# Performance work log

Measured on AMD Instinct MI355X. Metric: run time of the kernel, lower is better.

## Reference

```python
import jax, jax.numpy as jnp
import numpy as np
from jax import lax

D_MODEL = 512
D_STATE = 64
D_CONV = 4
EXPAND = 2
HEADDIM = 64
D_INNER = EXPAND * D_MODEL          # 1024
NHEADS = D_INNER // HEADDIM         # 16
CONV_DIM = D_INNER + 2 * D_STATE    # 1152 (x, B, C go through depthwise conv)
D_PROJ = 2 * D_INNER + 2 * D_STATE + NHEADS  # 2192
EPS = 1e-5


def silu(x):
    return x * jax.nn.sigmoid(x)


def layernorm(x, w, b):
    mu = jnp.mean(x, axis=-1, keepdims=True)
    var = jnp.mean((x - mu) ** 2, axis=-1, keepdims=True)
    return (x - mu) * lax.rsqrt(var + EPS) * w + b


def mamba2(x, in_w, conv_w, conv_b, dt_bias, A_log, D_h, mnorm_w, out_w):
    """Faithful Mamba2 forward (sequential selective-scan form of SSD).
    x: [B, L, D_MODEL]"""
    Bsz, L, _ = x.shape
    zxbcdt = x @ in_w  # [B, L, D_PROJ]
    z = zxbcdt[..., :D_INNER]
    xBC = zxbcdt[..., D_INNER:D_INNER + CONV_DIM]
    dt = zxbcdt[..., -NHEADS:]

    # causal depthwise conv1d over sequence, then SiLU
    xBC_pad = jnp.pad(xBC, ((0, 0), (D_CONV - 1, 0), (0, 0)))
    xBC = lax.conv_general_dilated(
        xBC_pad, conv_w, window_strides=(1,), padding='VALID',
        dimension_numbers=('NWC', 'WIO', 'NWC'), feature_group_count=CONV_DIM)
    xBC = silu(xBC + conv_b)

    xh = xBC[..., :D_INNER].reshape(Bsz, L, NHEADS, HEADDIM)      # [B,L,H,P]
    Bc = xBC[..., D_INNER:D_INNER + D_STATE]                      # [B,L,N]
    Cc = xBC[..., D_INNER + D_STATE:]                             # [B,L,N]

    dt = jax.nn.softplus(dt + dt_bias)          # [B,L,H]
    dA = jnp.exp(dt * (-jnp.exp(A_log)))        # [B,L,H]
    dtx = dt[..., None] * xh                    # [B,L,H,P]

    def step(h, ins):
        dA_t, dtx_t, B_t, C_t = ins  # [B,H], [B,H,P], [B,N], [B,N]
        h = h * dA_t[:, :, None, None] + dtx_t[..., None] * B_t[:, None, None, :]
        y = jnp.einsum('bhpn,bn->bhp', h, C_t)
        return h, y

    h0 = jnp.zeros((Bsz, NHEADS, HEADDIM, D_STATE), x.dtype)
    xs = (jnp.moveaxis(dA, 1, 0), jnp.moveaxis(dtx, 1, 0),
          jnp.moveaxis(Bc, 1, 0), jnp.moveaxis(Cc, 1, 0))
    _, ys = lax.scan(step, h0, xs)              # [L,B,H,P]
    y = jnp.moveaxis(ys, 0, 1) + D_h[None, None, :, None] * xh
    y = y.reshape(Bsz, L, D_INNER)

    # gated RMSNorm: rmsnorm(y * silu(z)) * weight
    g = y * silu(z)
    g = g * lax.rsqrt(jnp.mean(g * g, axis=-1, keepdims=True) + EPS) * mnorm_w
    return g @ out_w  # [B, L, D_MODEL]


def setup_inputs() -> dict:
    key = jax.random.key(0)
    ks = jax.random.split(key, 16)
    B, L = 2, 4096
    s = 0.02
    inp = {
        'x': jax.random.normal(ks[0], (B, L, D_MODEL), jnp.float32),
        'norm_in_w': jnp.ones((D_MODEL,), jnp.float32),
        'norm_in_b': jnp.zeros((D_MODEL,), jnp.float32),
        'norm_out_w': jnp.ones((D_MODEL,), jnp.float32),
        'norm_out_b': jnp.zeros((D_MODEL,), jnp.float32),
        'in_w': jax.random.normal(ks[1], (D_MODEL, D_PROJ), jnp.float32) * s,
        'conv_w': jax.random.normal(ks[2], (D_CONV, 1, CONV_DIM), jnp.float32) * 0.1,
        'conv_b': jnp.zeros((CONV_DIM,), jnp.float32),
        'dt_bias': jnp.log(jnp.expm1(jax.random.uniform(ks[3], (NHEADS,), jnp.float32, 0.001, 0.1))),
        'A_log': jnp.log(jnp.arange(1, NHEADS + 1, dtype=jnp.float32)),
        'D_h': jnp.ones((NHEADS,), jnp.float32),
        'mnorm_w': jnp.ones((D_INNER,), jnp.float32),
        'out_w': jax.random.normal(ks[4], (D_INNER, D_MODEL), jnp.float32) * s,
        'ff_w1': jax.random.normal(ks[5], (D_MODEL, 4 * D_MODEL), jnp.float32) * s,
        'ff_b1': jnp.zeros((4 * D_MODEL,), jnp.float32),
        'ff_w2': jax.random.normal(ks[6], (4 * D_MODEL, D_MODEL), jnp.float32) * s,
        'ff_b2': jnp.zeros((D_MODEL,), jnp.float32),
    }
    return inp


def reference(x, norm_in_w, norm_in_b, norm_out_w, norm_out_b, in_w, conv_w,
              conv_b, dt_bias, A_log, D_h, mnorm_w, out_w, ff_w1, ff_b1,
              ff_w2, ff_b2):
    xn = layernorm(x, norm_in_w, norm_in_b)
    fwd = mamba2(xn, in_w, conv_w, conv_b, dt_bias, A_log, D_h, mnorm_w, out_w)
    bwd = mamba2(jnp.flip(xn, axis=1), in_w, conv_w, conv_b, dt_bias, A_log,
                 D_h, mnorm_w, out_w)
    m = layernorm(fwd + jnp.flip(bwd, axis=1), norm_out_w, norm_out_b)
    ff = jax.nn.gelu(m @ ff_w1 + ff_b1, approximate=False) @ ff_w2 + ff_b2
    return ff + x
```

## Files before the change

kernel.cpp:

```cpp
#include <hip/hip_runtime.h>
#include <hip/hip_bf16.h>

#define LSEQ 4096
#define BSZ 2
#define DMODEL 512
#define DINNER 1024
#define DSTATE 64
#define NHEADS 16
#define CONVDIM 1152
#define DPROJ 2192
#define NPAD 2304
#define NTOK (BSZ*LSEQ)
#define NCH 64

typedef __attribute__((ext_vector_type(8))) short short8;
typedef __attribute__((ext_vector_type(4))) float f32x4;

__device__ inline unsigned short f2b(float v){
  unsigned int u = __builtin_bit_cast(unsigned int, v);
  unsigned int r = (u + 0x7FFFu + ((u >> 16) & 1u)) >> 16;
  return (unsigned short)r;
}
__device__ inline float b2f(unsigned short u){
  unsigned int x = ((unsigned int)u) << 16;
  return __builtin_bit_cast(float, x);
}
__device__ inline uint4 pack8(const float* v){
  uint4 pk;
  pk.x = (unsigned)f2b(v[0]) | ((unsigned)f2b(v[1])<<16);
  pk.y = (unsigned)f2b(v[2]) | ((unsigned)f2b(v[3])<<16);
  pk.z = (unsigned)f2b(v[4]) | ((unsigned)f2b(v[5])<<16);
  pk.w = (unsigned)f2b(v[6]) | ((unsigned)f2b(v[7])<<16);
  return pk;
}
__device__ inline float gelu_f(float x){
  float x2 = x*x;
  float u = x*(0.7978845608f + 0.0356774081f*x2);
  float au = fabsf(u);
  float z = __expf(-2.f*au);
  float t = (1.f - z)/(1.f + z);
  t = (u >= 0.f) ? t : -t;
  return 0.5f*x*(1.f + t);
}

#define GLL16(gp, lp) __builtin_amdgcn_global_load_lds( \
    (const __attribute__((address_space(1))) unsigned int*)(gp), \
    (__attribute__((address_space(3))) unsigned int*)(lp), 16, 0, 0)

__global__ __launch_bounds__(256) void wconv_t(const float* __restrict__ src,
    unsigned short* __restrict__ dst, int K, int Nsrc, int Npad){
  __shared__ float t[32][33];
  int n0 = blockIdx.x*32, k0 = blockIdx.y*32;
  int tx = threadIdx.x & 31, ty = threadIdx.x >> 5;
  for (int i=0;i<4;i++){
    int k = k0 + ty + i*8; int n = n0 + tx;
    t[ty + i*8][tx] = (n < Nsrc) ? src[(size_t)k*Nsrc + n] : 0.f;
  }
  __syncthreads();
  for (int i=0;i<4;i++){
    int n = n0 + ty + i*8; int k = k0 + tx;
    if (n < Npad) dst[(size_t)n*K + k] = f2b(t[tx][ty + i*8]);
  }
}

__global__ __launch_bounds__(256) void layernorm_k(const float* __restrict__ in,
    const float* __restrict__ w, const float* __restrict__ bb, unsigned short* __restrict__ out){
  int row = blockIdx.x; int tid = threadIdx.x;
  const float* r = in + (size_t)row*DMODEL;
  float v0 = r[tid], v1 = r[tid+256];
  float s = v0+v1, sq = v0*v0+v1*v1;
  for (int m=32;m>=1;m>>=1){ s += __shfl_xor(s,m); sq += __shfl_xor(sq,m); }
  __shared__ float ws_[4], wq_[4];
  int wave = tid>>6, lane = tid&63;
  if (lane==0){ ws_[wave]=s; wq_[wave]=sq; }
  __syncthreads();
  s = ws_[0]+ws_[1]+ws_[2]+ws_[3]; sq = wq_[0]+wq_[1]+wq_[2]+wq_[3];
  float mu = s * (1.f/DMODEL);
  float var = sq * (1.f/DMODEL) - mu*mu;
  float rs = rsqrtf(var + 1e-5f);
  out[(size_t)row*DMODEL + tid]     = f2b((v0-mu)*rs*w[tid] + bb[tid]);
  out[(size_t)row*DMODEL + tid+256] = f2b((v1-mu)*rs*w[tid+256] + bb[tid+256]);
}

__global__ __launch_bounds__(256) void gemm_k(const unsigned short* __restrict__ A,
    const unsigned short* __restrict__ Bt, void* __restrict__ outp,
    int M, int N, int K, int epi, const float* __restrict__ bias, const float* __restrict__ resid){
  __shared__ __align__(16) unsigned short smem[8320];
  unsigned short* As = smem;
  unsigned short* Bs = smem + 128*32;
  int tid = threadIdx.x;
  int lane = tid & 63, wave = tid >> 6;
  int wr = wave >> 1, wc = wave & 1;
  int l15 = lane & 15, q = lane >> 4;
  int bm = blockIdx.y, bn = blockIdx.x;
  f32x4 acc[4][4];
  for (int i=0;i<4;i++) for(int j=0;j<4;j++) acc[i][j] = (f32x4){0.f,0.f,0.f,0.f};
  const size_t abase = (size_t)bm*128*K;
  const size_t bbase = (size_t)bn*128*K;
  for (int k0 = 0; k0 < K; k0 += 32){
    #pragma unroll
    for (int i=0;i<2;i++){
      int idx = tid + i*256; int rr = idx>>2, cg = idx&3;
      GLL16(A  + abase + (size_t)rr*K + k0 + cg*8, As + idx*8);
      GLL16(Bt + bbase + (size_t)rr*K + k0 + cg*8, Bs + idx*8);
    }
    __syncthreads();
    short8 af[4], bfr[4];
    for (int mt=0;mt<4;mt++) af[mt]  = *(const short8*)(&As[(wr*64+mt*16+l15)*32 + q*8]);
    for (int nt=0;nt<4;nt++) bfr[nt] = *(const short8*)(&Bs[(wc*64+nt*16+l15)*32 + q*8]);
    for (int mt=0;mt<4;mt++)
      for (int nt=0;nt<4;nt++)
        acc[mt][nt] = __builtin_amdgcn_mfma_f32_16x16x32_bf16(af[mt], bfr[nt], acc[mt][nt], 0,0,0);
    __syncthreads();
  }
  float* cbuf = ((float*)smem) + wave*1040;
  int rbase = q*4;
  int gr0t = bm*128 + wr*64;
  int gc0 = bn*128 + wc*64;
  for (int mt=0; mt<4; mt++){
    for (int nt=0;nt<4;nt++)
      for (int rr=0;rr<4;rr++)
        cbuf[(rbase+rr)*65 + nt*16 + l15] = acc[mt][nt][rr];
    int gr0 = gr0t + mt*16;
    if (epi == 1 || epi == 3){
      int r8 = lane >> 3, c0 = (lane & 7)*8;
      #pragma unroll
      for (int h=0; h<2; h++){
        int row = h*8 + r8;
        float v[8];
        #pragma unroll
        for (int t=0;t<8;t++) v[t] = cbuf[row*65 + c0 + t];
        if (epi == 1){
          #pragma unroll
          for (int t=0;t<8;t++) v[t] = gelu_f(v[t] + bias[gc0 + c0 + t]);
        }
        *(uint4*)((unsigned short*)outp + (size_t)(gr0+row)*N + gc0 + c0) = pack8(v);
      }
    } else {
      int r4 = lane >> 4, c0 = (lane & 15)*4;
      #pragma unroll
      for (int h=0; h<4; h++){
        int row = h*4 + r4;
        float4 v;
        v.x = cbuf[row*65 + c0 + 0];
        v.y = cbuf[row*65 + c0 + 1];
        v.z = cbuf[row*65 + c0 + 2];
        v.w = cbuf[row*65 + c0 + 3];
        if (epi == 2){
          const float4 rv = *(const float4*)(resid + (size_t)(gr0+row)*N + gc0 + c0);
          v.x += bias[gc0+c0+0] + rv.x;
          v.y += bias[gc0+c0+1] + rv.y;
          v.z += bias[gc0+c0+2] + rv.z;
          v.w += bias[gc0+c0+3] + rv.w;
        }
        *(float4*)((float*)outp + (size_t)(gr0+row)*N + gc0 + c0) = v;
      }
    }
  }
}

__global__ __launch_bounds__(512, 2) void gemm256_k(const unsigned short* __restrict__ A,
    const unsigned short* __restrict__ Bt, unsigned short* __restrict__ outp,
    int M, int N, int K, int epi, const float* __restrict__ bias){
  __shared__ __align__(16) unsigned short As[32768];
  __shared__ __align__(16) unsigned short Bs[32768];
  const int tid = threadIdx.x;
  const int lane = tid & 63, wave = tid >> 6;
  const int wr = wave >> 2, wc = wave & 3;
  const int l15 = lane & 15, q = lane >> 4;
  int nbx = gridDim.x;
  int bid = blockIdx.y * nbx + blockIdx.x;
  int cpx = (nbx * gridDim.y) >> 3;
  int swz = (bid & 7) * cpx + (bid >> 3);
  int bn = swz % nbx, bm = swz / nbx;
  const int NT = K >> 6;
  const int j0 = tid, j1 = tid + 512;
  const int rr0 = j0 >> 2, rr1 = j1 >> 2;
  const int sc0 = (j0 & 3) ^ ((rr0 >> 1) & 3);
  const int sc1 = (j1 & 3) ^ ((rr1 >> 1) & 3);
  const unsigned short* a0 = A  + (size_t)(bm*256 + rr0)*K + sc0*8;
  const unsigned short* a1 = A  + (size_t)(bm*256 + rr1)*K + sc1*8;
  const unsigned short* b0 = Bt + (size_t)(bn*256 + rr0)*K + sc0*8;
  const unsigned short* b1 = Bt + (size_t)(bn*256 + rr1)*K + sc1*8;
  unsigned short* lA0 = As + j0*8;
  unsigned short* lA1 = As + j1*8;
  unsigned short* lB0 = Bs + j0*8;
  unsigned short* lB1 = Bs + j1*8;
#define STGA(t,kh) { const int go=(t)*64+(kh)*32, lo=((t)&1)*16384+(kh)*8192; \
  GLL16(a0+go, lA0+lo); GLL16(a1+go, lA1+lo); }
#define STGB(t,kh) { const int go=(t)*64+(kh)*32, lo=((t)&1)*16384+(kh)*8192; \
  GLL16(b0+go, lB0+lo); GLL16(b1+go, lB1+lo); }
  f32x4 acc[8][4];
  #pragma unroll
  for (int i=0;i<8;i++)
    #pragma unroll
    for (int j=0;j<4;j++) acc[i][j] = (f32x4){0.f,0.f,0.f,0.f};
  STGA(0,0); STGB(0,0); STGA(0,1); STGB(0,1);
  STGA(1,0); STGB(1,0);
  asm volatile("s_waitcnt vmcnt(4)" ::: "memory");
  __builtin_amdgcn_s_barrier();
  const int cOfs = (q ^ ((l15 >> 1) & 3)) * 8;
  const int arow = wr*128 + l15;
  const int brow = wc*64  + l15;
  for (int t = 0; t < NT; ++t){
    const unsigned short* Ab = As + (t & 1)*16384;
    const unsigned short* Bb = Bs + (t & 1)*16384;
    short8 af[4], bf4[4];
    #pragma unroll
    for (int mi=0;mi<4;mi++) af[mi]  = *(const short8*)(Ab + (arow + mi*16)*32 + cOfs);
    #pragma unroll
    for (int nt=0;nt<4;nt++) bf4[nt] = *(const short8*)(Bb + (brow + nt*16)*32 + cOfs);
    if (t+1 < NT) STGA(t+1,1);
    __builtin_amdgcn_s_barrier();
    asm volatile("s_waitcnt lgkmcnt(0)" ::: "memory");
    __builtin_amdgcn_sched_barrier(0);
    __builtin_amdgcn_s_setprio(1);
    #pragma unroll
    for (int mi=0;mi<4;mi++)
      #pragma unroll
      for (int nt=0;nt<4;nt++)
        acc[mi][nt] = __builtin_amdgcn_mfma_f32_16x16x32_bf16(af[mi], bf4[nt], acc[mi][nt], 0,0,0);
    __builtin_amdgcn_s_setprio(0);
    __builtin_amdgcn_s_barrier();
    #pragma unroll
    for (int mi=0;mi<4;mi++) af[mi] = *(const short8*)(Ab + (arow + (4+mi)*16)*32 + cOfs);
    if (t+1 < NT) STGB(t+1,1);
    __builtin_amdgcn_s_barrier();
    asm volatile("s_waitcnt lgkmcnt(0)" ::: "memory");
    __builtin_amdgcn_sched_barrier(0);
    __builtin_amdgcn_s_setprio(1);
    #pragma unroll
    for (int mi=0;mi<4;mi++)
      #pragma unroll
      for (int nt=0;nt<4;nt++)
        acc[4+mi][nt] = __builtin_amdgcn_mfma_f32_16x16x32_bf16(af[mi], bf4[nt], acc[4+mi][nt], 0,0,0);
    __builtin_amdgcn_s_setprio(0);
    __builtin_amdgcn_s_barrier();
    #pragma unroll
    for (int mi=0;mi<4;mi++) af[mi]  = *(const short8*)(Ab + 8192 + (arow + mi*16)*32 + cOfs);
    #pragma unroll
    for (int nt=0;nt<4;nt++) bf4[nt] = *(const short8*)(Bb + 8192 + (brow + nt*16)*32 + cOfs);
    if (t+2 < NT) STGA(t+2,0);
    __builtin_amdgcn_s_barrier();
    asm volatile("s_waitcnt lgkmcnt(0)" ::: "memory");
    __builtin_amdgcn_sched_barrier(0);
    __builtin_amdgcn_s_setprio(1);
    #pragma unroll
    for (int mi=0;mi<4;mi++)
      #pragma unroll
      for (int nt=0;nt<4;nt++)
        acc[mi][nt] = __builtin_amdgcn_mfma_f32_16x16x32_bf16(af[mi], bf4[nt], acc[mi][nt], 0,0,0);
    __builtin_amdgcn_s_setprio(0);
    __builtin_amdgcn_s_barrier();
    #pragma unroll
    for (int mi=0;mi<4;mi++) af[mi] = *(const short8*)(Ab + 8192 + (arow + (4+mi)*16)*32 + cOfs);
    if (t+2 < NT) STGB(t+2,0);
    __builtin_amdgcn_s_barrier();
    asm volatile("s_waitcnt lgkmcnt(0)" ::: "memory");
    __builtin_amdgcn_sched_barrier(0);
    __builtin_amdgcn_s_setprio(1);
    #pragma unroll
    for (int mi=0;mi<4;mi++)
      #pragma unroll
      for (int nt=0;nt<4;nt++)
        acc[4+mi][nt] = __builtin_amdgcn_mfma_f32_16x16x32_bf16(af[mi], bf4[nt], acc[4+mi][nt], 0,0,0);
    __builtin_amdgcn_s_setprio(0);
    if (t+2 < NT)      { asm volatile("s_waitcnt vmcnt(4)" ::: "memory"); }
    else if (t+1 < NT) { asm volatile("s_waitcnt vmcnt(0)" ::: "memory"); }
    __builtin_amdgcn_s_barrier();
  }
#undef STGA
#undef STGB
  float* cb = (float*)As + wave*1040;
  const int rbase = q*4;
  const int gr0t = bm*256 + wr*128;
  const int gc0 = bn*256 + wc*64;
  const int r8 = lane >> 3, c0 = (lane & 7)*8;
  #pragma unroll
  for (int mt=0; mt<8; mt++){
    #pragma unroll
    for (int nt=0;nt<4;nt++)
      #pragma unroll
      for (int r=0;r<4;r++)
        cb[(rbase+r)*65 + nt*16 + l15] = acc[mt][nt][r];
    int gr0 = gr0t + mt*16;
    #pragma unroll
    for (int h=0; h<2; h++){
      int row = h*8 + r8;
      float v[8];
      #pragma unroll
      for (int u=0;u<8;u++) v[u] = cb[row*65 + c0 + u];
      if (epi == 1){
        #pragma unroll
        for (int u=0;u<8;u++) v[u] = gelu_f(v[u] + bias[gc0 + c0 + u]);
      }
      *(uint4*)(outp + (size_t)(gr0+row)*N + gc0 + c0) = pack8(v);
    }
  }
}

__global__ __launch_bounds__(256) void dt_k(const unsigned short* __restrict__ zx,
    const float* __restrict__ dt_bias, const float* __restrict__ A_log,
    float* __restrict__ dAb, float* __restrict__ dtb){
  int b = blockIdx.y;
  int t = blockIdx.x*16 + (threadIdx.x>>4);
  int h = threadIdx.x & 15;
  float raw = b2f(zx[((size_t)b*LSEQ + t)*NPAD + (DINNER+CONVDIM) + h]) + dt_bias[h];
  float dt = (raw > 20.f) ? raw : log1pf(expf(raw));
  float dA = expf(-expf(A_log[h]) * dt);
  size_t f = ((size_t)b*LSEQ + t)*NHEADS + h;
  size_t r = ((size_t)(BSZ+b)*LSEQ + (LSEQ-1-t))*NHEADS + h;
  dAb[f] = dA; dtb[f] = dt;
  dAb[r] = dA; dtb[r] = dt;
}

__global__ __launch_bounds__(256) void conv_x_k(const unsigned short* __restrict__ zx,
    const float* __restrict__ conv_w, const float* __restrict__ conv_b,
    const float* __restrict__ dtb, unsigned short* __restrict__ dtxb,
    unsigned short* __restrict__ zcomp){
  int b = blockIdx.y;
  int t0blk = blockIdx.x * 32;
  int tid = threadIdx.x;
  int half = tid >> 7, cg = tid & 127;
  int c0 = cg * 8;
  int head = c0 >> 6;
  float wk[4][8], bias8[8];
  #pragma unroll
  for (int k=0;k<4;k++)
    #pragma unroll
    for (int j=0;j<8;j++) wk[k][j] = conv_w[k*CONVDIM + c0 + j];
  #pragma unroll
  for (int j=0;j<8;j++) bias8[j] = conv_b[c0 + j];
  __shared__ float sdtf[32][16], sdtb[32][16];
  for (int r = tid; r < 512; r += 256){
    int i = r >> 4, h = r & 15;
    sdtf[i][h] = dtb[((size_t)b*LSEQ + t0blk + i)*NHEADS + h];
    sdtb[i][h] = dtb[((size_t)(BSZ+b)*LSEQ + (LSEQ-1-(t0blk+i)))*NHEADS + h];
  }
  __syncthreads();
  int t0 = t0blk + half*16;
  float w0[8],w1[8],w2[8],w3[8];
  #pragma unroll
  for (int j=0;j<8;j++){ w1[j]=0.f; w2[j]=0.f; w3[j]=0.f; }
  for (int it=0; it<22; ++it){
    int t = t0 - 3 + it;
    #pragma unroll
    for (int j=0;j<8;j++){ w0[j]=w1[j]; w1[j]=w2[j]; w2[j]=w3[j]; }
    if (t >= 0 && t < LSEQ){
      uint4 xv = *(const uint4*)(zx + ((size_t)b*LSEQ + t)*NPAD + DINNER + c0);
      const unsigned short* xs = (const unsigned short*)&xv;
      #pragma unroll
      for (int j=0;j<8;j++) w3[j] = b2f(xs[j]);
      if (t >= t0 && t < t0+16){
        uint4 zv = *(const uint4*)(zx + ((size_t)b*LSEQ + t)*NPAD + c0);
        *(uint4*)(zcomp + ((size_t)b*LSEQ + t)*DINNER + c0) = zv;
      }
    } else {
      #pragma unroll
      for (int j=0;j<8;j++) w3[j] = 0.f;
    }
    if (t >= t0 && t < t0+16){
      float dtf = sdtf[t - t0blk][head];
      float v[8];
      #pragma unroll
      for (int j=0;j<8;j++){
        float a = bias8[j] + wk[0][j]*w0[j] + wk[1][j]*w1[j] + wk[2][j]*w2[j] + wk[3][j]*w3[j];
        v[j] = (a / (1.f + expf(-a))) * dtf;
      }
      *(uint4*)(dtxb + ((size_t)b*LSEQ + t)*DINNER + c0) = pack8(v);
    }
    int tau = t - 3;
    if (tau >= t0 && tau < t0+16){
      float dtv = sdtb[tau - t0blk][head];
      float v[8];
      #pragma unroll
      for (int j=0;j<8;j++){
        float a = bias8[j] + wk[0][j]*w3[j] + wk[1][j]*w2[j] + wk[2][j]*w1[j] + wk[3][j]*w0[j];
        v[j] = (a / (1.f + expf(-a))) * dtv;
      }
      *(uint4*)(dtxb + ((size_t)(BSZ+b)*LSEQ + (LSEQ-1-tau))*DINNER + c0) = pack8(v);
    }
  }
}

__global__ __launch_bounds__(256) void conv_bc_k(const unsigned short* __restrict__ zx,
    const float* __restrict__ conv_w, const float* __restrict__ conv_b,
    unsigned short* __restrict__ Bb, unsigned short* __restrict__ Cb){
  int b = blockIdx.y;
  int t0blk = blockIdx.x * 64;
  int tid = threadIdx.x;
  int slot = tid >> 4, cg = tid & 15;
  int c0 = cg*8;
  int ccol = DINNER + 1024 + c0;
  int cw = 1024 + c0;
  float wk[4][8], bias8[8];
  #pragma unroll
  for (int k=0;k<4;k++)
    #pragma unroll
    for (int j=0;j<8;j++) wk[k][j] = conv_w[k*CONVDIM + cw + j];
  #pragma unroll
  for (int j=0;j<8;j++) bias8[j] = conv_b[cw + j];
  int t0 = t0blk + slot*4;
  float w0[8],w1[8],w2[8],w3[8];
  #pragma unroll
  for (int j=0;j<8;j++){ w1[j]=0.f; w2[j]=0.f; w3[j]=0.f; }
  for (int it=0; it<10; ++it){
    int t = t0 - 3 + it;
    #pragma unroll
    for (int j=0;j<8;j++){ w0[j]=w1[j]; w1[j]=w2[j]; w2[j]=w3[j]; }
    if (t >= 0 && t < LSEQ){
      uint4 xv = *(const uint4*)(zx + ((size_t)b*LSEQ + t)*NPAD + ccol);
      const unsigned short* xs = (const unsigned short*)&xv;
      #pragma unroll
      for (int j=0;j<8;j++) w3[j] = b2f(xs[j]);
    } else {
      #pragma unroll
      for (int j=0;j<8;j++) w3[j] = 0.f;
    }
    if (t >= t0 && t < t0+4){
      float v[8];
      #pragma unroll
      for (int j=0;j<8;j++){
        float a = bias8[j] + wk[0][j]*w0[j] + wk[1][j]*w1[j] + wk[2][j]*w2[j] + wk[3][j]*w3[j];
        v[j] = a / (1.f + expf(-a));
      }
      size_t tok = (size_t)b*LSEQ + t;
      if (c0 < 64) *(uint4*)(Bb + tok*DSTATE + c0)      = pack8(v);
      else         *(uint4*)(Cb + tok*DSTATE + (c0-64)) = pack8(v);
    }
    int tau = t - 3;
    if (tau >= t0 && tau < t0+4){
      float v[8];
      #pragma unroll
      for (int j=0;j<8;j++){
        float a = bias8[j] + wk[0][j]*w3[j] + wk[1][j]*w2[j] + wk[2][j]*w1[j] + wk[3][j]*w0[j];
        v[j] = a / (1.f + expf(-a));
      }
      size_t tok = (size_t)(BSZ+b)*LSEQ + (LSEQ-1-tau);
      if (c0 < 64) *(uint4*)(Bb + tok*DSTATE + c0)      = pack8(v);
      else         *(uint4*)(Cb + tok*DSTATE + (c0-64)) = pack8(v);
    }
  }
}

__device__ inline void gemm64(const unsigned short* Ab, const unsigned short* Bb_,
                              int l15, int q, f32x4 acc[4][4]){
  #pragma unroll
  for (int ks=0; ks<2; ks++){
    short8 af[4], bf4[4];
    #pragma unroll
    for (int mt=0;mt<4;mt++) af[mt]  = *(const short8*)(Ab  + (mt*16+l15)*72 + ks*32 + q*8);
    #pragma unroll
    for (int nt=0;nt<4;nt++) bf4[nt] = *(const short8*)(Bb_ + (nt*16+l15)*72 + ks*32 + q*8);
    #pragma unroll
    for (int mt=0;mt<4;mt++)
      #pragma unroll
      for (int nt=0;nt<4;nt++)
        acc[mt][nt] = __builtin_amdgcn_mfma_f32_16x16x32_bf16(af[mt], bf4[nt], acc[mt][nt], 0,0,0);
  }
}

__global__ __launch_bounds__(64) void ssd1_k(const float* __restrict__ dAb,
    const unsigned short* __restrict__ dtxb, const unsigned short* __restrict__ Bb,
    const unsigned short* __restrict__ Cb,
    unsigned short* __restrict__ y0, unsigned short* __restrict__ y1,
    unsigned short* __restrict__ hbuf, float* __restrict__ Pch, float* __restrict__ ebuf){
  int ch = blockIdx.x, h = blockIdx.y, z = blockIdx.z;
  int d = z >> 1, b = z & 1;
  int lane = threadIdx.x;
  int l15 = lane & 15, q = lane >> 4;
  int tr = lane >> 3, cb8 = (lane & 7)*8;
  size_t tokb = (size_t)z*LSEQ + (size_t)ch*64;
  size_t zhc = ((size_t)z*NHEADS + h)*NCH + ch;
  __shared__ __align__(16) unsigned short S1[64*72];
  __shared__ __align__(16) unsigned short S2[64*72];
  __shared__ __align__(16) unsigned short S3[64*72];
  __shared__ float Lb[64];
  float L = fmaxf(logf(dAb[(tokb + lane)*NHEADS + h]), -60.f);
  #pragma unroll
  for (int off=1; off<64; off<<=1){
    float v = __shfl_up(L, off);
    if (lane >= off) L += v;
  }
  Lb[lane] = L;
  float e = expf(L);
  ebuf[zhc*64 + lane] = e;
  if (lane == 63) Pch[zhc] = e;
  for (int i=0;i<8;i++){
    int t = i*8 + tr;
    *(uint4*)&S1[t*72 + cb8] = *(const uint4*)(Cb + (tokb+t)*DSTATE + cb8);
    *(uint4*)&S2[t*72 + cb8] = *(const uint4*)(Bb + (tokb+t)*DSTATE + cb8);
    uint4 xv = *(const uint4*)(dtxb + (tokb+t)*DINNER + (size_t)h*64 + cb8);
    const unsigned short* xs = (const unsigned short*)&xv;
    #pragma unroll
    for (int j=0;j<8;j++) S3[(cb8+j)*72 + t] = xs[j];
  }
  f32x4 sa[4][4];
  for (int i=0;i<4;i++) for (int j=0;j<4;j++) sa[i][j] = (f32x4){0.f,0.f,0.f,0.f};
  gemm64(S1, S2, l15, q, sa);
  float Lsv[4];
  #pragma unroll
  for (int nt=0;nt<4;nt++) Lsv[nt] = Lb[nt*16 + l15];
  #pragma unroll
  for (int mt=0;mt<4;mt++){
    #pragma unroll
    for (int r=0;r<4;r++){
      int t = mt*16 + q*4 + r;
      float Lt = Lb[t];
      #pragma unroll
      for (int nt=0;nt<4;nt++){
        int s = nt*16 + l15;
        float v = (t >= s) ? expf(Lt - Lsv[nt]) * sa[mt][nt][r] : 0.f;
        S1[t*72 + s] = f2b(v);
      }
    }
  }
  f32x4 ya[4][4];
  for (int i=0;i<4;i++) for (int j=0;j<4;j++) ya[i][j] = (f32x4){0.f,0.f,0.f,0.f};
  gemm64(S1, S3, l15, q, ya);
  #pragma unroll
  for (int mt=0;mt<4;mt++)
    #pragma unroll
    for (int pt=0;pt<4;pt++)
      #pragma unroll
      for (int r=0;r<4;r++)
        S2[(mt*16+q*4+r)*72 + pt*16 + l15] = f2b(ya[mt][pt][r]);
  unsigned short* yb = d ? y1 : y0;
  for (int i=0;i<8;i++){
    int t = i*8 + tr; int g = ch*64 + t;
    int tph = d ? (LSEQ-1-g) : g;
    *(uint4*)(yb + ((size_t)b*LSEQ + tph)*DINNER + (size_t)h*64 + cb8) = *(uint4*)&S2[t*72 + cb8];
  }
  float L63 = Lb[63];
  for (int i=0;i<8;i++){
    int s = i*8 + tr;
    float w = expf(L63 - Lb[s]);
    uint4 bv = *(const uint4*)(Bb + (tokb+s)*DSTATE + cb8);
    const unsigned short* bs = (const unsigned short*)&bv;
    #pragma unroll
    for (int j=0;j<8;j++) S2[(cb8+j)*72 + s] = f2b(w * b2f(bs[j]));
  }
  f32x4 ga[4][4];
  for (int i=0;i<4;i++) for (int j=0;j<4;j++) ga[i][j] = (f32x4){0.f,0.f,0.f,0.f};
  gemm64(S3, S2, l15, q, ga);
  #pragma unroll
  for (int pt=0;pt<4;pt++)
    #pragma unroll
    for (int nt=0;nt<4;nt++)
      #pragma unroll
      for (int r=0;r<4;r++)
        S1[(pt*16+q*4+r)*72 + nt*16 + l15] = f2b(ga[pt][nt][r]);
  for (int i=0;i<8;i++){
    int p = i*8 + tr;
    *(uint4*)(hbuf + zhc*4096 + (size_t)p*64 + cb8) = *(uint4*)&S1[p*72 + cb8];
  }
}

__global__ __launch_bounds__(256) void comb_k(unsigned short* __restrict__ hbuf,
    const float* __restrict__ Pch){
  int u = blockIdx.x; int tid = threadIdx.x;
  int kb = blockIdx.y * 4;
  float hreg[4];
  #pragma unroll
  for (int k=0;k<4;k++) hreg[k]=0.f;
  for (int ch=0; ch<NCH; ch++){
    size_t base = ((size_t)u*NCH + ch)*4096;
    float P = Pch[(size_t)u*NCH + ch];
    #pragma unroll
    for (int k=0;k<4;k++){
      size_t idx = base + tid + (size_t)(kb+k)*256;
      float t = b2f(hbuf[idx]);
      hbuf[idx] = f2b(hreg[k]);
      hreg[k] = hreg[k]*P + t;
    }
  }
}

__global__ __launch_bounds__(64) void ssd2_k(const unsigned short* __restrict__ Cb,
    const unsigned short* __restrict__ hbuf, const unsigned short* __restrict__ dtxb,
    const float* __restrict__ dtb, const float* __restrict__ ebuf, const float* __restrict__ Dh,
    unsigned short* __restrict__ y0, unsigned short* __restrict__ y1){
  int ch = blockIdx.x, h = blockIdx.y, z = blockIdx.z;
  int d = z >> 1, b = z & 1;
  int lane = threadIdx.x;
  int l15 = lane & 15, q = lane >> 4;
  int tr = lane >> 3, cb8 = (lane & 7)*8;
  size_t tokb = (size_t)z*LSEQ + (size_t)ch*64;
  size_t zhc = ((size_t)z*NHEADS + h)*NCH + ch;
  __shared__ __align__(16) unsigned short S1[64*72];
  __shared__ __align__(16) unsigned short S2[64*72];
  __shared__ __align__(16) unsigned short S3[64*72];
  __shared__ float eb2[64], dti[64];
  eb2[lane] = ebuf[zhc*64 + lane];
  dti[lane] = 1.f / dtb[(tokb + lane)*NHEADS + h];
  float Dv = Dh[h];
  for (int i=0;i<8;i++){
    int t = i*8 + tr;
    *(uint4*)&S1[t*72 + cb8] = *(const uint4*)(Cb + (tokb+t)*DSTATE + cb8);
    *(uint4*)&S2[t*72 + cb8] = *(const uint4*)(hbuf + zhc*4096 + (size_t)t*64 + cb8);
  }
  f32x4 acc[4][4];
  for (int i=0;i<4;i++) for (int j=0;j<4;j++) acc[i][j] = (f32x4){0.f,0.f,0.f,0.f};
  gemm64(S1, S2, l15, q, acc);
  unsigned short* yb = d ? y1 : y0;
  #pragma unroll
  for (int mt=0;mt<4;mt++){
    #pragma unroll
    for (int r=0;r<4;r++){
      int t = mt*16 + q*4 + r; int g = ch*64 + t;
      int tph = d ? (LSEQ-1-g) : g;
      size_t rowb = ((size_t)b*LSEQ + tph)*DINNER + (size_t)h*64;
      size_t dxb_ = (tokb + t)*DINNER + (size_t)h*64;
      float et = eb2[t], di = dti[t];
      #pragma unroll
      for (int pt=0;pt<4;pt++){
        int p = pt*16 + l15;
        float v = acc[mt][pt][r]*et + b2f(yb[rowb + p]) + Dv * b2f(dtxb[dxb_ + p]) * di;
        S3[t*72 + p] = f2b(v);
      }
    }
  }
  for (int i=0;i<8;i++){
    int t = i*8 + tr; int g = ch*64 + t;
    int tph = d ? (LSEQ-1-g) : g;
    *(uint4*)(yb + ((size_t)b*LSEQ + tph)*DINNER + (size_t)h*64 + cb8) = *(uint4*)&S3[t*72 + cb8];
  }
}

__global__ __launch_bounds__(256) void gate_k(const unsigned short* __restrict__ y0,
    const unsigned short* __restrict__ y1, const unsigned short* __restrict__ zcomp,
    const float* __restrict__ mnw, unsigned short* __restrict__ gsum){
  int tok = blockIdx.x; int tid = threadIdx.x;
  __shared__ float g0s[DINNER], g1s[DINNER];
  float ss0 = 0.f, ss1 = 0.f;
  for (int i=0;i<4;i++){
    int c = tid + i*256;
    float z = b2f(zcomp[(size_t)tok*DINNER + c]);
    float sz = z / (1.f + expf(-z));
    float g0 = b2f(y0[(size_t)tok*DINNER + c]) * sz;
    float g1 = b2f(y1[(size_t)tok*DINNER + c]) * sz;
    g0s[c] = g0; g1s[c] = g1;
    ss0 += g0*g0; ss1 += g1*g1;
  }
  for (int m=32;m>=1;m>>=1){ ss0 += __shfl_xor(ss0,m); ss1 += __shfl_xor(ss1,m); }
  __shared__ float w0[4], w1[4];
  int wave = tid>>6, lane = tid&63;
  if (lane==0){ w0[wave]=ss0; w1[wave]=ss1; }
  __syncthreads();
  ss0 = w0[0]+w0[1]+w0[2]+w0[3];
  ss1 = w1[0]+w1[1]+w1[2]+w1[3];
  float r0 = rsqrtf(ss0*(1.f/DINNER) + 1e-5f);
  float r1 = rsqrtf(ss1*(1.f/DINNER) + 1e-5f);
  for (int i=0;i<4;i++){
    int c = tid + i*256;
    gsum[(size_t)tok*DINNER + c] = f2b((g0s[c]*r0 + g1s[c]*r1) * mnw[c]);
  }
}

extern "C" void kernel_launch(void* const* d_in, const int* in_sizes, int n_in,
                              void* d_out, int out_size, void* d_ws, size_t ws_size,
                              hipStream_t stream){
  const float* x       = (const float*)d_in[0];
  const float* nin_w   = (const float*)d_in[1];
  const float* nin_b   = (const float*)d_in[2];
  const float* nout_w  = (const float*)d_in[3];
  const float* nout_b  = (const float*)d_in[4];
  const float* in_w    = (const float*)d_in[5];
  const float* conv_w  = (const float*)d_in[6];
  const float* conv_b  = (const float*)d_in[7];
  const float* dt_bias = (const float*)d_in[8];
  const float* A_log   = (const float*)d_in[9];
  const float* D_h     = (const float*)d_in[10];
  const float* mnorm_w = (const float*)d_in[11];
  const float* out_w   = (const float*)d_in[12];
  const float* ff_w1   = (const float*)d_in[13];
  const float* ff_b1   = (const float*)d_in[14];
  const float* ff_w2   = (const float*)d_in[15];
  const float* ff_b2   = (const float*)d_in[16];
  float* out = (float*)d_out;

  char* ws = (char*)d_ws;
  size_t off = 0;
  auto alloc = [&](size_t bytes)->char*{
    char* p = ws + off; off = (off + bytes + 255) & ~(size_t)255; return p; };
  unsigned short* xn_bf = (unsigned short*)alloc((size_t)NTOK*DMODEL*2);
  unsigned short* in_wT = (unsigned short*)alloc((size_t)NPAD*DMODEL*2);
  unsigned short* out_wT= (unsigned short*)alloc((size_t)DMODEL*DINNER*2);
  unsigned short* w1T   = (unsigned short*)alloc((size_t)2048*DMODEL*2);
  unsigned short* w2T   = (unsigned short*)alloc((size_t)DMODEL*2048*2);
  unsigned short* zx    = (unsigned short*)alloc((size_t)NTOK*NPAD*2);
  unsigned short* zcomp = (unsigned short*)alloc((size_t)NTOK*DINNER*2);
  float*          dAb   = (float*)alloc((size_t)2*NTOK*NHEADS*4);
  float*          dtb   = (float*)alloc((size_t)2*NTOK*NHEADS*4);
  unsigned short* Bb    = (unsigned short*)alloc((size_t)2*NTOK*DSTATE*2);
  unsigned short* Cb    = (unsigned short*)alloc((size_t)2*NTOK*DSTATE*2);
  unsigned short* dtxb  = (unsigned short*)alloc((size_t)2*NTOK*DINNER*2);
  unsigned short* y0    = (unsigned short*)alloc((size_t)NTOK*DINNER*2);
  unsigned short* y1    = (unsigned short*)alloc((size_t)NTOK*DINNER*2);
  float*          Pch   = (float*)alloc((size_t)64*NCH*4);
  float*          ebuf  = (float*)alloc((size_t)64*NCH*64*4);
  size_t need = off;
  if (need > ws_size) return;

  unsigned short* hbuf  = zx;
  unsigned short* gsum  = dtxb;
  float* mpre = (float*)(dtxb + (size_t)NTOK*DINNER);
  unsigned short* m_bf  = y0;
  unsigned short* h1    = zx;

  wconv_t<<<dim3(NPAD/32,   DMODEL/32), 256, 0, stream>>>(in_w,  in_wT,  DMODEL, DPROJ,  NPAD);
  wconv_t<<<dim3(DMODEL/32, DINNER/32), 256, 0, stream>>>(out_w, out_wT, DINNER, DMODEL, DMODEL);
  wconv_t<<<dim3(2048/32,   DMODEL/32), 256, 0, stream>>>(ff_w1, w1T,    DMODEL, 2048,   2048);
  wconv_t<<<dim3(DMODEL/32, 2048/32),   256, 0, stream>>>(ff_w2, w2T,    2048,   DMODEL, DMODEL);
  layernorm_k<<<NTOK, 256, 0, stream>>>(x, nin_w, nin_b, xn_bf);
  gemm256_k<<<dim3(NPAD/256, NTOK/256), 512, 0, stream>>>(xn_bf, in_wT, zx, NTOK, NPAD, DMODEL, 3, nullptr);
  dt_k<<<dim3(LSEQ/16, BSZ), 256, 0, stream>>>(zx, dt_bias, A_log, dAb, dtb);
  conv_x_k<<<dim3(LSEQ/32, BSZ), 256, 0, stream>>>(zx, conv_w, conv_b, dtb, dtxb, zcomp);
  conv_bc_k<<<dim3(LSEQ/64, BSZ), 256, 0, stream>>>(zx, conv_w, conv_b, Bb, Cb);
  ssd1_k<<<dim3(NCH, NHEADS, 2*BSZ), 64, 0, stream>>>(dAb, dtxb, Bb, Cb, y0, y1, hbuf, Pch, ebuf);
  comb_k<<<dim3(64, 4), 256, 0, stream>>>(hbuf, Pch);
  ssd2_k<<<dim3(NCH, NHEADS, 2*BSZ), 64, 0, stream>>>(Cb, hbuf, dtxb, dtb, ebuf, D_h, y0, y1);
  gate_k<<<NTOK, 256, 0, stream>>>(y0, y1, zcomp, mnorm_w, gsum);
  gemm_k<<<dim3(DMODEL/128, NTOK/128), 256, 0, stream>>>(gsum, out_wT, mpre, NTOK, DMODEL, DINNER, 0, nullptr, nullptr);
  layernorm_k<<<NTOK, 256, 0, stream>>>(mpre, nout_w, nout_b, m_bf);
  gemm256_k<<<dim3(2048/256, NTOK/256), 512, 0, stream>>>(m_bf, w1T, h1, NTOK, 2048, DMODEL, 1, ff_b1);
  gemm_k<<<dim3(DMODEL/128, NTOK/128), 256, 0, stream>>>(h1, w2T, out, NTOK, DMODEL, 2048, 2, ff_b2, x);
}
```

Baseline: 429.6 us.

## Replace small-tile GEMMs with split-K 256-tile GEMM plus reduction kernels

Removes the 128x128 gemm_k and routes the out-projection and FF2 GEMMs (N=512) through the larger 256x256 pipelined kernel, splitting K across blockIdx.z (2 and 4 ways) so there are enough blocks to fill the device. Partial fp32 results are written to reused scratch buffers. They are summed inside a new two-input layernorm for the out-projection and by a reduce kernel that also adds bias and the residual for FF2. This trades extra fp32 partial-sum traffic and two added reduction passes for better MFMA efficiency and occupancy on the narrow GEMMs.

```diff
diff --git a/kernel.cpp b/kernel.cpp
--- a/kernel.cpp
+++ b/kernel.cpp
@@ -82,86 +82,51 @@
   out[(size_t)row*DMODEL + tid+256] = f2b((v1-mu)*rs*w[tid+256] + bb[tid+256]);
 }
 
-__global__ __launch_bounds__(256) void gemm_k(const unsigned short* __restrict__ A,
-    const unsigned short* __restrict__ Bt, void* __restrict__ outp,
-    int M, int N, int K, int epi, const float* __restrict__ bias, const float* __restrict__ resid){
-  __shared__ __align__(16) unsigned short smem[8320];
-  unsigned short* As = smem;
-  unsigned short* Bs = smem + 128*32;
-  int tid = threadIdx.x;
-  int lane = tid & 63, wave = tid >> 6;
-  int wr = wave >> 1, wc = wave & 1;
-  int l15 = lane & 15, q = lane >> 4;
-  int bm = blockIdx.y, bn = blockIdx.x;
-  f32x4 acc[4][4];
-  for (int i=0;i<4;i++) for(int j=0;j<4;j++) acc[i][j] = (f32x4){0.f,0.f,0.f,0.f};
-  const size_t abase = (size_t)bm*128*K;
-  const size_t bbase = (size_t)bn*128*K;
-  for (int k0 = 0; k0 < K; k0 += 32){
-    #pragma unroll
-    for (int i=0;i<2;i++){
-      int idx = tid + i*256; int rr = idx>>2, cg = idx&3;
-      GLL16(A  + abase + (size_t)rr*K + k0 + cg*8, As + idx*8);
-      GLL16(Bt + bbase + (size_t)rr*K + k0 + cg*8, Bs + idx*8);
-    }
-    __syncthreads();
-    short8 af[4], bfr[4];
-    for (int mt=0;mt<4;mt++) af[mt]  = *(const short8*)(&As[(wr*64+mt*16+l15)*32 + q*8]);
-    for (int nt=0;nt<4;nt++) bfr[nt] = *(const short8*)(&Bs[(wc*64+nt*16+l15)*32 + q*8]);
-    for (int mt=0;mt<4;mt++)
-      for (int nt=0;nt<4;nt++)
-        acc[mt][nt] = __builtin_amdgcn_mfma_f32_16x16x32_bf16(af[mt], bfr[nt], acc[mt][nt], 0,0,0);
-    __syncthreads();
-  }
-  float* cbuf = ((float*)smem) + wave*1040;
-  int rbase = q*4;
-  int gr0t = bm*128 + wr*64;
-  int gc0 = bn*128 + wc*64;
-  for (int mt=0; mt<4; mt++){
-    for (int nt=0;nt<4;nt++)
-      for (int rr=0;rr<4;rr++)
-        cbuf[(rbase+rr)*65 + nt*16 + l15] = acc[mt][nt][rr];
-    int gr0 = gr0t + mt*16;
-    if (epi == 1 || epi == 3){
-      int r8 = lane >> 3, c0 = (lane & 7)*8;
-      #pragma unroll
-      for (int h=0; h<2; h++){
-        int row = h*8 + r8;
-        float v[8];
-        #pragma unroll
-        for (int t=0;t<8;t++) v[t] = cbuf[row*65 + c0 + t];
-        if (epi == 1){
-          #pragma unroll
-          for (int t=0;t<8;t++) v[t] = gelu_f(v[t] + bias[gc0 + c0 + t]);
-        }
-        *(uint4*)((unsigned short*)outp + (size_t)(gr0+row)*N + gc0 + c0) = pack8(v);
-      }
-    } else {
-      int r4 = lane >> 4, c0 = (lane & 15)*4;
-      #pragma unroll
-      for (int h=0; h<4; h++){
-        int row = h*4 + r4;
-        float4 v;
-        v.x = cbuf[row*65 + c0 + 0];
-        v.y = cbuf[row*65 + c0 + 1];
-        v.z = cbuf[row*65 + c0 + 2];
-        v.w = cbuf[row*65 + c0 + 3];
-        if (epi == 2){
-          const float4 rv = *(const float4*)(resid + (size_t)(gr0+row)*N + gc0 + c0);
-          v.x += bias[gc0+c0+0] + rv.x;
-          v.y += bias[gc0+c0+1] + rv.y;
-          v.z += bias[gc0+c0+2] + rv.z;
-          v.w += bias[gc0+c0+3] + rv.w;
-        }
-        *(float4*)((float*)outp + (size_t)(gr0+row)*N + gc0 + c0) = v;
-      }
-    }
+__global__ __launch_bounds__(256) void layernorm2_k(const float* __restrict__ in0,
+    const float* __restrict__ in1,
+    const float* __restrict__ w, const float* __restrict__ bb, unsigned short* __restrict__ out){
+  int row = blockIdx.x; int tid = threadIdx.x;
+  const float* r0 = in0 + (size_t)row*DMODEL;
+  const float* r1 = in1 + (size_t)row*DMODEL;
+  float v0 = r0[tid] + r1[tid], v1 = r0[tid+256] + r1[tid+256];
+  float s = v0+v1, sq = v0*v0+v1*v1;
+  for (int m=32;m>=1;m>>=1){ s += __shfl_xor(s,m); sq += __shfl_xor(sq,m); }
+  __shared__ float ws_[4], wq_[4];
+  int wave = tid>>6, lane = tid&63;
+  if (lane==0){ ws_[wave]=s; wq_[wave]=sq; }
+  __syncthreads();
+  s = ws_[0]+ws_[1]+ws_[2]+ws_[3]; sq = wq_[0]+wq_[1]+wq_[2]+wq_[3];
+  float mu = s * (1.f/DMODEL);
+  float var = sq * (1.f/DMODEL) - mu*mu;
+  float rs = rsqrtf(var + 1e-5f);
+  out[(size_t)row*DMODEL + tid]     = f2b((v0-mu)*rs*w[tid] + bb[tid]);
+  out[(size_t)row*DMODEL + tid+256] = f2b((v1-mu)*rs*w[tid+256] + bb[tid+256]);
+}
+
+__global__ __launch_bounds__(256) void reduce4_k(const float* __restrict__ pa,
+    const float* __restrict__ pb, const float* __restrict__ bias,
+    const float* __restrict__ resid, float* __restrict__ out){
+  const size_t MN4 = (size_t)NTOK*DMODEL/4;
+  for (size_t i = (size_t)blockIdx.x*256 + threadIdx.x; i < MN4; i += (size_t)gridDim.x*256){
+    float4 a0 = ((const float4*)pa)[i];
+    float4 a1 = ((const float4*)pa)[i + MN4];
+    float4 b0 = ((const float4*)pb)[i];
+    float4 b1 = ((const float4*)pb)[i + MN4];
+    float4 rv = ((const float4*)resid)[i];
+    int col = (int)((i*4) & (DMODEL-1));
+    const float4 bs = *(const float4*)(bias + col);
+    float4 o;
+    o.x = a0.x + a1.x + b0.x + b1.x + bs.x + rv.x;
+    o.y = a0.y + a1.y + b0.y + b1.y + bs.y + rv.y;
+    o.z = a0.z + a1.z + b0.z + b1.z + bs.z + rv.z;
+    o.w = a0.w + a1.w + b0.w + b1.w + bs.w + rv.w;
+    ((float4*)out)[i] = o;
   }
 }
 
 __global__ __launch_bounds__(512, 2) void gemm256_k(const unsigned short* __restrict__ A,
-    const unsigned short* __restrict__ Bt, unsigned short* __restrict__ outp,
-    int M, int N, int K, int epi, const float* __restrict__ bias){
+    const unsigned short* __restrict__ Bt, void* __restrict__ outp, void* __restrict__ outp_hi,
+    int M, int N, int K, int klen, int epi, const float* __restrict__ bias){
   __shared__ __align__(16) unsigned short As[32768];
   __shared__ __align__(16) unsigned short Bs[32768];
   const int tid = threadIdx.x;
@@ -173,15 +138,16 @@
   int cpx = (nbx * gridDim.y) >> 3;
   int swz = (bid & 7) * cpx + (bid >> 3);
   int bn = swz % nbx, bm = swz / nbx;
-  const int NT = K >> 6;
+  const int kstart = blockIdx.z * klen;
+  const int NT = klen >> 6;
   const int j0 = tid, j1 = tid + 512;
   const int rr0 = j0 >> 2, rr1 = j1 >> 2;
   const int sc0 = (j0 & 3) ^ ((rr0 >> 1) & 3);
   const int sc1 = (j1 & 3) ^ ((rr1 >> 1) & 3);
-  const unsigned short* a0 = A  + (size_t)(bm*256 + rr0)*K + sc0*8;
-  const unsigned short* a1 = A  + (size_t)(bm*256 + rr1)*K + sc1*8;
-  const unsigned short* b0 = Bt + (size_t)(bn*256 + rr0)*K + sc0*8;
-  const unsigned short* b1 = Bt + (size_t)(bn*256 + rr1)*K + sc1*8;
+  const unsigned short* a0 = A  + (size_t)(bm*256 + rr0)*K + kstart + sc0*8;
+  const unsigned short* a1 = A  + (size_t)(bm*256 + rr1)*K + kstart + sc1*8;
+  const unsigned short* b0 = Bt + (size_t)(bn*256 + rr0)*K + kstart + sc0*8;
+  const unsigned short* b1 = Bt + (size_t)(bn*256 + rr1)*K + kstart + sc1*8;
   unsigned short* lA0 = As + j0*8;
   unsigned short* lA1 = As + j1*8;
   unsigned short* lB0 = Bs + j0*8;
@@ -275,7 +241,6 @@
   const int rbase = q*4;
   const int gr0t = bm*256 + wr*128;
   const int gc0 = bn*256 + wc*64;
-  const int r8 = lane >> 3, c0 = (lane & 7)*8;
   #pragma unroll
   for (int mt=0; mt<8; mt++){
     #pragma unroll
@@ -284,17 +249,34 @@
       for (int r=0;r<4;r++)
         cb[(rbase+r)*65 + nt*16 + l15] = acc[mt][nt][r];
     int gr0 = gr0t + mt*16;
-    #pragma unroll
-    for (int h=0; h<2; h++){
-      int row = h*8 + r8;
-      float v[8];
-      #pragma unroll
-      for (int u=0;u<8;u++) v[u] = cb[row*65 + c0 + u];
-      if (epi == 1){
+    if (epi == 0){
+      float* po = (float*)((blockIdx.z < 2) ? outp : outp_hi)
+                + (size_t)(blockIdx.z & 1) * ((size_t)M * N);
+      int r4 = lane >> 4, c0f = (lane & 15)*4;
+      #pragma unroll
+      for (int h=0; h<4; h++){
+        int row = h*4 + r4;
+        float4 v;
+        v.x = cb[row*65 + c0f + 0];
+        v.y = cb[row*65 + c0f + 1];
+        v.z = cb[row*65 + c0f + 2];
+        v.w = cb[row*65 + c0f + 3];
+        *(float4*)(po + (size_t)(gr0+row)*N + gc0 + c0f) = v;
+      }
+    } else {
+      int r8 = lane >> 3, c0 = (lane & 7)*8;
+      #pragma unroll
+      for (int h=0; h<2; h++){
+        int row = h*8 + r8;
+        float v[8];
         #pragma unroll
-        for (int u=0;u<8;u++) v[u] = gelu_f(v[u] + bias[gc0 + c0 + u]);
-      }
-      *(uint4*)(outp + (size_t)(gr0+row)*N + gc0 + c0) = pack8(v);
+        for (int u=0;u<8;u++) v[u] = cb[row*65 + c0 + u];
+        if (epi == 1){
+          #pragma unroll
+          for (int u=0;u<8;u++) v[u] = gelu_f(v[u] + bias[gc0 + c0 + u]);
+        }
+        *(uint4*)((unsigned short*)outp + (size_t)(gr0+row)*N + gc0 + c0) = pack8(v);
+      }
     }
   }
 }
@@ -704,16 +686,18 @@
 
   unsigned short* hbuf  = zx;
   unsigned short* gsum  = dtxb;
-  float* mpre = (float*)(dtxb + (size_t)NTOK*DINNER);
   unsigned short* m_bf  = y0;
   unsigned short* h1    = zx;
+  float* mp   = (float*)zx;
+  float* fp01 = (float*)dtxb;
+  float* fp23 = (float*)y0;
 
   wconv_t<<<dim3(NPAD/32,   DMODEL/32), 256, 0, stream>>>(in_w,  in_wT,  DMODEL, DPROJ,  NPAD);
   wconv_t<<<dim3(DMODEL/32, DINNER/32), 256, 0, stream>>>(out_w, out_wT, DINNER, DMODEL, DMODEL);
   wconv_t<<<dim3(2048/32,   DMODEL/32), 256, 0, stream>>>(ff_w1, w1T,    DMODEL, 2048,   2048);
   wconv_t<<<dim3(DMODEL/32, 2048/32),   256, 0, stream>>>(ff_w2, w2T,    2048,   DMODEL, DMODEL);
   layernorm_k<<<NTOK, 256, 0, stream>>>(x, nin_w, nin_b, xn_bf);
-  gemm256_k<<<dim3(NPAD/256, NTOK/256), 512, 0, stream>>>(xn_bf, in_wT, zx, NTOK, NPAD, DMODEL, 3, nullptr);
+  gemm256_k<<<dim3(NPAD/256, NTOK/256, 1), 512, 0, stream>>>(xn_bf, in_wT, zx, nullptr, NTOK, NPAD, DMODEL, DMODEL, 3, nullptr);
   dt_k<<<dim3(LSEQ/16, BSZ), 256, 0, stream>>>(zx, dt_bias, A_log, dAb, dtb);
   conv_x_k<<<dim3(LSEQ/32, BSZ), 256, 0, stream>>>(zx, conv_w, conv_b, dtb, dtxb, zcomp);
   conv_bc_k<<<dim3(LSEQ/64, BSZ), 256, 0, stream>>>(zx, conv_w, conv_b, Bb, Cb);
@@ -721,8 +705,9 @@
   comb_k<<<dim3(64, 4), 256, 0, stream>>>(hbuf, Pch);
   ssd2_k<<<dim3(NCH, NHEADS, 2*BSZ), 64, 0, stream>>>(Cb, hbuf, dtxb, dtb, ebuf, D_h, y0, y1);
   gate_k<<<NTOK, 256, 0, stream>>>(y0, y1, zcomp, mnorm_w, gsum);
-  gemm_k<<<dim3(DMODEL/128, NTOK/128), 256, 0, stream>>>(gsum, out_wT, mpre, NTOK, DMODEL, DINNER, 0, nullptr, nullptr);
-  layernorm_k<<<NTOK, 256, 0, stream>>>(mpre, nout_w, nout_b, m_bf);
-  gemm256_k<<<dim3(2048/256, NTOK/256), 512, 0, stream>>>(m_bf, w1T, h1, NTOK, 2048, DMODEL, 1, ff_b1);
-  gemm_k<<<dim3(DMODEL/128, NTOK/128), 256, 0, stream>>>(h1, w2T, out, NTOK, DMODEL, 2048, 2, ff_b2, x);
-}
+  gemm256_k<<<dim3(DMODEL/256, NTOK/256, 2), 512, 0, stream>>>(gsum, out_wT, mp, nullptr, NTOK, DMODEL, DINNER, 512, 0, nullptr);
+  layernorm2_k<<<NTOK, 256, 0, stream>>>(mp, mp + (size_t)NTOK*DMODEL, nout_w, nout_b, m_bf);
+  gemm256_k<<<dim3(2048/256, NTOK/256, 1), 512, 0, stream>>>(m_bf, w1T, h1, nullptr, NTOK, 2048, DMODEL, DMODEL, 1, ff_b1);
+  gemm256_k<<<dim3(DMODEL/256, NTOK/256, 4), 512, 0, stream>>>(h1, w2T, fp01, fp23, NTOK, DMODEL, 2048, 512, 0, nullptr);
+  reduce4_k<<<2048, 256, 0, stream>>>(fp01, fp23, ff_b2, x, out);
+}
```

Result: faster. 419.8 us (-2.3%).
